# Kernel tuning notes

Measured on AMD Instinct MI355X. Metric: run time of the kernel, lower is better.

## Reference

```python
import jax, jax.numpy as jnp
import numpy as np

B, S = 2, 1024
V, H = 32000, 1024
NH, NKV = 16, 8
HD = H // NH          # 64
L = 8
I = 4 * H             # 4096
EPS = 1e-6
THETA = 10000.0
NEG = -1e9


def setup_inputs() -> dict:
    key = jax.random.key(0)
    ks = jax.random.split(key, 12)
    std = 0.02
    f = lambda k, shape: jax.random.normal(k, shape, jnp.float32) * std
    return {
        "input_ids": jax.random.randint(ks[0], (B, S), 0, V, dtype=jnp.int32),
        "embed": f(ks[1], (V, H)),
        "Wq": f(ks[2], (L, H, NH * HD)),
        "Wk": f(ks[3], (L, H, NKV * HD)),
        "Wv": f(ks[4], (L, H, NKV * HD)),
        "Wo": f(ks[5], (L, NH * HD, H)),
        "Wg": f(ks[6], (L, H, I)),
        "Wu": f(ks[7], (L, H, I)),
        "Wd": f(ks[8], (L, I, H)),
        "ln1": jnp.ones((L, H), jnp.float32),
        "ln2": jnp.ones((L, H), jnp.float32),
        "norm_w": jnp.ones((H,), jnp.float32),
        "lm_head": f(ks[9], (H, V)),
    }


def _rmsnorm(x, w):
    var = jnp.mean(x * x, axis=-1, keepdims=True)
    return x * jax.lax.rsqrt(var + EPS) * w


def _rotate_half(x):
    x1, x2 = jnp.split(x, 2, axis=-1)
    return jnp.concatenate((-x2, x1), axis=-1)


def reference(input_ids, embed, Wq, Wk, Wv, Wo, Wg, Wu, Wd, ln1, ln2, norm_w, lm_head):
    # RoPE tables [S, HD] (freqs duplicated, matching cat((freqs, freqs)))
    inv_freq = 1.0 / (THETA ** (jnp.arange(0, HD, 2, dtype=jnp.float32) / HD))
    t = jnp.arange(S, dtype=jnp.float32)
    freqs = t[:, None] * inv_freq[None, :]
    emb = jnp.concatenate((freqs, freqs), axis=-1)
    cos = jnp.cos(emb)[None, None]  # [1,1,S,HD]
    sin = jnp.sin(emb)[None, None]
    # causal mask [S, S]
    mask = jnp.where(jnp.tril(jnp.ones((S, S), bool)), 0.0, NEG).astype(jnp.float32)

    def layer(h, p):
        wq, wk, wv, wo, wg, wu, wd, g1, g2 = p
        x = _rmsnorm(h, g1)
        q = (x @ wq).reshape(B, S, NH, HD).transpose(0, 2, 1, 3)   # [B,NH,S,HD]
        k = (x @ wk).reshape(B, S, NKV, HD).transpose(0, 2, 1, 3)  # [B,NKV,S,HD]
        v = (x @ wv).reshape(B, S, NKV, HD).transpose(0, 2, 1, 3)
        q = q * cos + _rotate_half(q) * sin
        k = k * cos + _rotate_half(k) * sin
        rep = NH // NKV
        k = jnp.repeat(k, rep, axis=1)  # GQA repeat_interleave
        v = jnp.repeat(v, rep, axis=1)
        scores = jnp.einsum("bhqd,bhkd->bhqk", q, k) / np.sqrt(HD) + mask
        probs = jax.nn.softmax(scores, axis=-1)
        o = jnp.einsum("bhqk,bhkd->bhqd", probs, v)
        o = o.transpose(0, 2, 1, 3).reshape(B, S, NH * HD)
        h = h + o @ wo
        x = _rmsnorm(h, g2)
        h = h + (jax.nn.silu(x @ wg) * (x @ wu)) @ wd
        return h, None

    h = embed[input_ids]  # [B,S,H]
    h, _ = jax.lax.scan(layer, h, (Wq, Wk, Wv, Wo, Wg, Wu, Wd, ln1, ln2))
    h = _rmsnorm(h, norm_w)
    return h @ lm_head  # logits [B,S,V]
```

## Files before the change

### kernel.cpp

```cpp
#include <hip/hip_runtime.h>


typedef unsigned short u16;
typedef __bf16  bf16x8 __attribute__((ext_vector_type(8)));
typedef unsigned short u16x8 __attribute__((ext_vector_type(8)));
typedef float   f32x4  __attribute__((ext_vector_type(4)));

#define DEV static __device__ __forceinline__

constexpr int NB  = 2;
constexpr int S   = 1024;
constexpr int NT  = NB * S;
constexpr int H   = 1024;
constexpr int NH  = 16;
constexpr int NKV = 8;
constexpr int HD  = 64;
constexpr int NL  = 8;
constexpr int FF  = 4096;
constexpr int V   = 32000;
constexpr int QKVW = 2048;

DEV float b2f(u16 x) { return __uint_as_float(((unsigned)x) << 16); }
DEV u16   f2b(float f) {
  unsigned i = __float_as_uint(f);
  return (u16)((i + 0x7fffu + ((i >> 16) & 1u)) >> 16);
}

DEV void gload16(const void* g, void* l) {
  __builtin_amdgcn_global_load_lds(
      (const __attribute__((address_space(1))) void*)g,
      (__attribute__((address_space(3))) void*)l, 16, 0, 0);
}

DEV bf16x8 ld128(const u16* p) { return *reinterpret_cast<const bf16x8*>(p); }

template <int EPI>
__global__ __launch_bounds__(512, 2) void gemm256_k(
    const u16* __restrict__ A, int lda,
    const u16* __restrict__ Bt, int ldb,
    void* __restrict__ C, int ldc, int K)
{
  __shared__ __align__(16) u16 Asm[4][256 * 32];
  __shared__ __align__(16) u16 Bsm[4][256 * 32];

  const int tid  = threadIdx.x;
  const int lane = tid & 63;
  const int lrow = lane & 15;
  const int g    = lane >> 4;
  const int wid  = tid >> 6;
  const int wm   = wid >> 2, wn = wid & 3;

  int flat = blockIdx.y * gridDim.x + blockIdx.x;
  const int cpx = (gridDim.x * gridDim.y) >> 3;
  flat = (flat & 7) * cpx + (flat >> 3);
  const int bx = flat % gridDim.x;
  const int by = flat / gridDim.x;

  const int r0   = tid >> 2, pp = tid & 3;
  const int row1 = 128 + (tid >> 2);
  const int p0 = pp ^ ((r0 ^ (r0 >> 2)) & 3);
  const int p1 = pp ^ ((row1 ^ (row1 >> 2)) & 3);
  const u16* aS0 = A  + (size_t)(bx * 256 + r0)   * lda + p0 * 8;
  const u16* aS1 = A  + (size_t)(bx * 256 + row1) * lda + p1 * 8;
  const u16* bS0 = Bt + (size_t)(by * 256 + r0)   * ldb + p0 * 8;
  const u16* bS1 = Bt + (size_t)(by * 256 + row1) * ldb + p1 * 8;
  const int aB0 = tid * 16, aB1 = (512 + tid) * 16;

  int aOff[8], bOff[4];
  #pragma unroll
  for (int fm = 0; fm < 8; fm++) {
    const int r = wm * 128 + fm * 16 + lrow;
    aOff[fm] = r * 32 + (g ^ ((r ^ (r >> 2)) & 3)) * 8;
  }
  #pragma unroll
  for (int fn = 0; fn < 4; fn++) {
    const int r = wn * 64 + fn * 16 + lrow;
    bOff[fn] = r * 32 + (g ^ ((r ^ (r >> 2)) & 3)) * 8;
  }

  f32x4 acc[8][4] = {};
  const int ntk = K / 32;

  #pragma unroll
  for (int ts = 0; ts < 3; ts++) {
    const long kt = (long)ts * 32;
    gload16(aS0 + kt, (char*)Asm[ts] + aB0);
    gload16(bS0 + kt, (char*)Bsm[ts] + aB0);
    gload16(aS1 + kt, (char*)Asm[ts] + aB1);
    gload16(bS1 + kt, (char*)Bsm[ts] + aB1);
  }
  asm volatile("s_waitcnt vmcnt(8)" ::: "memory");
  __builtin_amdgcn_s_barrier();

#define KTILE(VMW, STG)                                                         \
  {                                                                             \
    const int rs = t & 3, ss = (t + 3) & 3;                                     \
    const long kt = (long)(t + 3) * 32;                                         \
    bf16x8 af[4], bf[4];                                                        \
    _Pragma("unroll") for (int i = 0; i < 4; i++) bf[i] = ld128(&Bsm[rs][bOff[i]]); \
    _Pragma("unroll") for (int i = 0; i < 4; i++) af[i] = ld128(&Asm[rs][aOff[i]]); \
    if (STG) { gload16(aS0 + kt, (char*)Asm[ss] + aB0);                         \
               gload16(bS0 + kt, (char*)Bsm[ss] + aB0); }                       \
    __builtin_amdgcn_s_barrier();                                               \
    asm volatile("s_waitcnt lgkmcnt(0)" ::: "memory");                          \
    __builtin_amdgcn_sched_barrier(0);                                          \
    __builtin_amdgcn_s_setprio(1);                                              \
    _Pragma("unroll") for (int m = 0; m < 4; m++)                               \
      _Pragma("unroll") for (int n = 0; n < 4; n++)                             \
        acc[m][n] = __builtin_amdgcn_mfma_f32_16x16x32_bf16(af[m], bf[n], acc[m][n], 0, 0, 0); \
    __builtin_amdgcn_s_setprio(0);                                              \
    __builtin_amdgcn_s_barrier();                                               \
    _Pragma("unroll") for (int i = 0; i < 4; i++) af[i] = ld128(&Asm[rs][aOff[4 + i]]); \
    if (STG) { gload16(aS1 + kt, (char*)Asm[ss] + aB1);                         \
               gload16(bS1 + kt, (char*)Bsm[ss] + aB1); }                       \
    __builtin_amdgcn_s_barrier();                                               \
    asm volatile("s_waitcnt lgkmcnt(0)" ::: "memory");                          \
    __builtin_amdgcn_sched_barrier(0);                                          \
    __builtin_amdgcn_s_setprio(1);                                              \
    _Pragma("unroll") for (int m = 0; m < 4; m++)                               \
      _Pragma("unroll") for (int n = 0; n < 4; n++)                             \
        acc[4 + m][n] = __builtin_amdgcn_mfma_f32_16x16x32_bf16(af[m], bf[n], acc[4 + m][n], 0, 0, 0); \
    __builtin_amdgcn_s_setprio(0);                                              \
    VMW;                                                                        \
    __builtin_amdgcn_sched_barrier(0);                                          \
    __builtin_amdgcn_s_barrier();                                               \
  }

  {
    int t = 0;
    for (; t < ntk - 3; ++t) KTILE(asm volatile("s_waitcnt vmcnt(8)" ::: "memory"), true);
    KTILE(asm volatile("s_waitcnt vmcnt(4)" ::: "memory"), false); ++t;
    KTILE(asm volatile("s_waitcnt vmcnt(0)" ::: "memory"), false); ++t;
    KTILE((void)0, false);
  }
#undef KTILE

  if (EPI == 2) {
    #pragma unroll
    for (int fm = 0; fm < 8; fm++) {
      #pragma unroll
      for (int fp = 0; fp < 2; fp++) {
        #pragma unroll
        for (int r = 0; r < 4; r++) {
          const size_t row = bx * 256 + wm * 128 + fm * 16 + g * 4 + r;
          const int nb = by * 256 + wn * 64 + fp * 32;
          const int oc = (nb >> 5) * 16 + lrow;
          const float gg = acc[fm][2 * fp][r];
          const float uu = acc[fm][2 * fp + 1][r];
          ((u16*)C)[row * ldc + oc] = f2b(gg / (1.f + __expf(-gg)) * uu);
        }
      }
    }
  } else {
    #pragma unroll
    for (int fm = 0; fm < 8; fm++) {
      #pragma unroll
      for (int fn = 0; fn < 4; fn++) {
        #pragma unroll
        for (int r = 0; r < 4; r++) {
          const size_t row = bx * 256 + wm * 128 + fm * 16 + g * 4 + r;
          const size_t col = by * 256 + wn * 64 + fn * 16 + lrow;
          ((float*)C)[row * ldc + col] = acc[fm][fn][r];
        }
      }
    }
  }
}

template <int BM, int BN, int WM, int WN, int EPI>
__global__ __launch_bounds__(256) void gemm_k(
    const u16* __restrict__ A, int lda,
    const u16* __restrict__ Bt, int ldb,
    void* __restrict__ C, int ldc,
    const float2* __restrict__ tab, int K)
{
  __shared__ __align__(16) u16 As[BM * 32];
  __shared__ __align__(16) u16 Bs[BN * 32];

  const int tid  = threadIdx.x;
  const int lane = tid & 63;
  const int lrow = lane & 15;
  const int kb   = lane >> 4;
  const int w    = tid >> 6;
  const int wm   = w / WN, wn = w % WN;
  constexpr int WR = BM / WM, WC = BN / WN;
  constexpr int FM = WR / 16, FN = WC / 16;

  const u16* Ap = A + blockIdx.x * BM * lda;
  const u16* Bp = Bt + blockIdx.y * BN * ldb;

  f32x4 acc[FM][FN] = {};

  for (int k0 = 0; k0 < K; k0 += 32) {
    #pragma unroll
    for (int i = 0; i < (BM * 4) / 256; i++) {
      const int c = i * 256 + tid;
      gload16(Ap + (c >> 2) * lda + k0 + (c & 3) * 8, (char*)As + c * 16);
    }
    #pragma unroll
    for (int i = 0; i < (BN * 4) / 256; i++) {
      const int c = i * 256 + tid;
      gload16(Bp + (c >> 2) * ldb + k0 + (c & 3) * 8, (char*)Bs + c * 16);
    }
    __syncthreads();

    bf16x8 af[FM], bfv[FN];
    #pragma unroll
    for (int fm = 0; fm < FM; fm++)
      af[fm] = *reinterpret_cast<const bf16x8*>(As + (wm * WR + fm * 16 + lrow) * 32 + kb * 8);
    #pragma unroll
    for (int fn = 0; fn < FN; fn++)
      bfv[fn] = *reinterpret_cast<const bf16x8*>(Bs + (wn * WC + fn * 16 + lrow) * 32 + kb * 8);

    #pragma unroll
    for (int fm = 0; fm < FM; fm++) {
      #pragma unroll
      for (int fn = 0; fn < FN; fn++) {
        acc[fm][fn] = __builtin_amdgcn_mfma_f32_16x16x32_bf16(af[fm], bfv[fn], acc[fm][fn], 0, 0, 0);
      }
    }
    __syncthreads();
  }

  if (EPI == 4) {
    const int colb = blockIdx.y * BN + wn * WC;
    const int head = colb >> 6;
    const float qs = (head < 16) ? 0.125f : 1.0f;
    #pragma unroll
    for (int fm = 0; fm < FM; fm++) {
      #pragma unroll
      for (int r = 0; r < 4; r++) {
        const int row = blockIdx.x * BM + wm * WR + fm * 16 + kb * 4 + r;
        if (head >= 24) {
          #pragma unroll
          for (int fn = 0; fn < FN; fn++)
            ((u16*)C)[row * ldc + colb + fn * 16 + lrow] = f2b(acc[fm][fn][r]);
        } else {
          const int s = row & (S - 1);
          #pragma unroll
          for (int fp = 0; fp < 2; fp++) {
            const int d = fp * 16 + lrow;
            const float2 cs = tab[s * 32 + d];
            const float x1 = acc[fm][fp][r];
            const float x2 = acc[fm][fp + 2][r];
            ((u16*)C)[row * ldc + colb + d]      = f2b((x1 * cs.x - x2 * cs.y) * qs);
            ((u16*)C)[row * ldc + colb + d + 32] = f2b((x2 * cs.x + x1 * cs.y) * qs);
          }
        }
      }
    }
  } else {
    #pragma unroll
    for (int fm = 0; fm < FM; fm++) {
      #pragma unroll
      for (int fn = 0; fn < FN; fn++) {
        #pragma unroll
        for (int r = 0; r < 4; r++) {
          const int row = blockIdx.x * BM + wm * WR + fm * 16 + kb * 4 + r;
          const int col = blockIdx.y * BN + wn * WC + fn * 16 + lrow;
          ((u16*)C)[row * ldc + col] = f2b(acc[fm][fn][r]);
        }
      }
    }
  }
}

__global__ __launch_bounds__(256) void transpose_k(
    const float* __restrict__ W, u16* __restrict__ WT, int K, int N, int rmode,
    size_t wstride, size_t tstride)
{
  __shared__ float t[32][33];
  const float* Wp = W + (size_t)blockIdx.z * wstride;
  u16* WTp = WT + (size_t)blockIdx.z * tstride;
  const int k0 = blockIdx.x * 32, n0 = blockIdx.y * 32;
  const int tx = threadIdx.x & 31, ty = threadIdx.x >> 5;
  #pragma unroll
  for (int i = 0; i < 32; i += 8)
    t[ty + i][tx] = Wp[(size_t)(k0 + ty + i) * N + (n0 + tx)];
  __syncthreads();
  #pragma unroll
  for (int i = 0; i < 32; i += 8) {
    const int n = n0 + ty + i;
    const int orow = (rmode == 0) ? n : ((n >> 4) * 32 + (n & 15) + ((rmode == 2) ? 16 : 0));
    WTp[(size_t)orow * K + (k0 + tx)] = f2b(t[tx][ty + i]);
  }
}

__global__ __launch_bounds__(256) void embed_k(
    const int* __restrict__ ids, const float* __restrict__ E, float* __restrict__ h)
{
  const int t = blockIdx.x;
  const int id = ids[t];
  ((float4*)(h + t * H))[threadIdx.x] = ((const float4*)(E + (size_t)id * H))[threadIdx.x];
}

__global__ __launch_bounds__(256) void rmsnorm_k(
    const float* __restrict__ h, const float* __restrict__ w, u16* __restrict__ x)
{
  const int row = blockIdx.x;
  const float4 hv = ((const float4*)(h + row * H))[threadIdx.x];
  float s = hv.x * hv.x + hv.y * hv.y + hv.z * hv.z + hv.w * hv.w;
  #pragma unroll
  for (int off = 32; off; off >>= 1) s += __shfl_xor(s, off, 64);
  __shared__ float red[4];
  if ((threadIdx.x & 63) == 0) red[threadIdx.x >> 6] = s;
  __syncthreads();
  s = red[0] + red[1] + red[2] + red[3];
  const float scale = rsqrtf(s * (1.f / H) + 1e-6f);
  const float4 wv = ((const float4*)w)[threadIdx.x];
  ushort4 ov;
  ov.x = f2b(hv.x * scale * wv.x);
  ov.y = f2b(hv.y * scale * wv.y);
  ov.z = f2b(hv.z * scale * wv.z);
  ov.w = f2b(hv.w * scale * wv.w);
  ((ushort4*)(x + row * H))[threadIdx.x] = ov;
}

__global__ __launch_bounds__(256) void addnorm_k(
    float* __restrict__ h, const u16* __restrict__ dl,
    const float* __restrict__ w, u16* __restrict__ x)
{
  const int row = blockIdx.x;
  float4 hv = ((const float4*)(h + row * H))[threadIdx.x];
  const ushort4 dv = ((const ushort4*)(dl + row * H))[threadIdx.x];
  hv.x += b2f(dv.x); hv.y += b2f(dv.y); hv.z += b2f(dv.z); hv.w += b2f(dv.w);
  ((float4*)(h + row * H))[threadIdx.x] = hv;
  float s = hv.x * hv.x + hv.y * hv.y + hv.z * hv.z + hv.w * hv.w;
  #pragma unroll
  for (int off = 32; off; off >>= 1) s += __shfl_xor(s, off, 64);
  __shared__ float red[4];
  if ((threadIdx.x & 63) == 0) red[threadIdx.x >> 6] = s;
  __syncthreads();
  s = red[0] + red[1] + red[2] + red[3];
  const float scale = rsqrtf(s * (1.f / H) + 1e-6f);
  const float4 wv = ((const float4*)w)[threadIdx.x];
  ushort4 ov;
  ov.x = f2b(hv.x * scale * wv.x);
  ov.y = f2b(hv.y * scale * wv.y);
  ov.z = f2b(hv.z * scale * wv.z);
  ov.w = f2b(hv.w * scale * wv.w);
  ((ushort4*)(x + row * H))[threadIdx.x] = ov;
}

__global__ __launch_bounds__(256) void ropetab_k(float2* __restrict__ tab)
{
  const int idx = blockIdx.x * 256 + threadIdx.x;
  const int s = idx >> 5, d = idx & 31;
  const float ang = s * powf(10000.f, -(2.f * d) / 64.f);
  float sn, cs;
  sincosf(ang, &sn, &cs);
  tab[idx] = make_float2(cs, sn);
}

__global__ __launch_bounds__(256) void fattn_k(
    const u16* __restrict__ qkv, u16* __restrict__ o)
{
  __shared__ __align__(16) u16 Ks[64 * 64];
  __shared__ __align__(16) u16 Vt[64 * 72];
  __shared__ __align__(16) u16 Pw[4][16 * 64];

  const int tid  = threadIdx.x;
  const int lane = tid & 63;
  const int lrow = lane & 15;
  const int g    = lane >> 4;
  const int w    = tid >> 6;

  const int bid = blockIdx.x;
  const int j   = bid >> 3;
  const int bh  = (bid & 7) * 4 + (j & 3);
  const int bx  = 15 - (j >> 2);
  const int b = bh >> 4, hh = bh & 15, kh = hh >> 1;
  const int q0 = bx * 64;

  bf16x8 aq[2];
  {
    const int qrow = q0 + w * 16 + lrow;
    const u16* qp = qkv + (size_t)(b * S + qrow) * QKVW + hh * 64 + g * 8;
    aq[0] = *reinterpret_cast<const bf16x8*>(qp);
    aq[1] = *reinterpret_cast<const bf16x8*>(qp + 32);
  }

  f32x4 oacc[4] = {};
  float mrow[4], lsum[4];
  #pragma unroll
  for (int r = 0; r < 4; r++) { mrow[r] = -1e30f; lsum[r] = 0.f; }

  const int nt = bx + 1;
  for (int t = 0; t < nt; t++) {
    const int kv0 = t * 64;
    __syncthreads();

    #pragma unroll
    for (int i = 0; i < 2; i++) {
      const int c = i * 256 + tid;
      const int r = c >> 3, p = c & 7;
      gload16(qkv + (size_t)(b * S + kv0 + r) * QKVW + 1024 + kh * 64 + ((p ^ (r & 7)) * 8),
              (char*)Ks + c * 16);
    }
    u16x8 vreg[2];
    #pragma unroll
    for (int i = 0; i < 2; i++) {
      const int c = i * 256 + tid;
      const int k = c >> 3, dch = c & 7;
      vreg[i] = *reinterpret_cast<const u16x8*>(
          qkv + (size_t)(b * S + kv0 + k) * QKVW + 1536 + kh * 64 + dch * 8);
    }
    #pragma unroll
    for (int i = 0; i < 2; i++) {
      const int c = i * 256 + tid;
      const int k = c >> 3, d0 = (c & 7) * 8;
      #pragma unroll
      for (int j2 = 0; j2 < 8; j2++) {
        const int d = d0 + j2;
        Vt[d * 72 + (((k >> 3) ^ (d >> 3)) * 8) + (k & 7)] = vreg[i][j2];
      }
    }
    __syncthreads();

    f32x4 sacc[4] = {};
    #pragma unroll
    for (int n = 0; n < 4; n++) {
      const int row = n * 16 + lrow;
      #pragma unroll
      for (int k2 = 0; k2 < 2; k2++) {
        const bf16x8 bk = *reinterpret_cast<const bf16x8*>(
            Ks + row * 64 + (((k2 * 4 + g) ^ (row & 7)) * 8));
        sacc[n] = __builtin_amdgcn_mfma_f32_16x16x32_bf16(aq[k2], bk, sacc[n], 0, 0, 0);
      }
    }

    float rmv[4];
    #pragma unroll
    for (int r = 0; r < 4; r++) {
      const int qglob = q0 + w * 16 + g * 4 + r;
      float rm = -1e30f;
      #pragma unroll
      for (int n = 0; n < 4; n++) {
        const int kg = kv0 + n * 16 + lrow;
        if (kg > qglob) sacc[n][r] = -1e30f;
        rm = fmaxf(rm, sacc[n][r]);
      }
      #pragma unroll
      for (int mk = 1; mk < 16; mk <<= 1) rm = fmaxf(rm, __shfl_xor(rm, mk, 64));
      rmv[r] = rm;
    }

    int need = 0;
    #pragma unroll
    for (int r = 0; r < 4; r++) need |= (rmv[r] > mrow[r] + 8.f) ? 1 : 0;
    if (__any(need)) {
      #pragma unroll
      for (int r = 0; r < 4; r++) {
        const float mnew  = fmaxf(mrow[r], rmv[r]);
        const float scale = __expf(mrow[r] - mnew);
        mrow[r] = mnew;
        lsum[r] *= scale;
        #pragma unroll
        for (int dt = 0; dt < 4; dt++) oacc[dt][r] *= scale;
      }
    }

    #pragma unroll
    for (int r = 0; r < 4; r++) {
      float rs = 0.f;
      u16 pb[4];
      #pragma unroll
      for (int n = 0; n < 4; n++) {
        const float p = __expf(sacc[n][r] - mrow[r]);
        rs += p;
        pb[n] = f2b(p);
      }
      #pragma unroll
      for (int mk = 1; mk < 16; mk <<= 1) rs += __shfl_xor(rs, mk, 64);
      lsum[r] += rs;
      const int ql = g * 4 + r;
      #pragma unroll
      for (int n = 0; n < 4; n++) {
        const int k = n * 16 + lrow;
        Pw[w][ql * 64 + (((k >> 3) ^ (ql & 7)) * 8) + (k & 7)] = pb[n];
      }
    }

    #pragma unroll
    for (int k2 = 0; k2 < 2; k2++) {
      const bf16x8 pa = *reinterpret_cast<const bf16x8*>(
          &Pw[w][lrow * 64 + (((k2 * 4 + g) ^ (lrow & 7)) * 8)]);
      #pragma unroll
      for (int dt = 0; dt < 4; dt++) {
        const int d = dt * 16 + lrow;
        const bf16x8 vb = *reinterpret_cast<const bf16x8*>(
            &Vt[d * 72 + (((k2 * 4 + g) ^ (d >> 3)) * 8)]);
        oacc[dt] = __builtin_amdgcn_mfma_f32_16x16x32_bf16(pa, vb, oacc[dt], 0, 0, 0);
      }
    }
  }

  #pragma unroll
  for (int dt = 0; dt < 4; dt++) {
    #pragma unroll
    for (int r = 0; r < 4; r++) {
      const int qrow = q0 + w * 16 + g * 4 + r;
      o[(size_t)(b * S + qrow) * H + hh * 64 + dt * 16 + lrow] =
          f2b(oacc[dt][r] / lsum[r]);
    }
  }
}

extern "C" void kernel_launch(void* const* d_in, const int* in_sizes, int n_in,
                              void* d_out, int out_size, void* d_ws, size_t ws_size,
                              hipStream_t stream)
{
  const int*   ids  = (const int*)d_in[0];
  const float* EW   = (const float*)d_in[1];
  const float* Wq   = (const float*)d_in[2];
  const float* Wk   = (const float*)d_in[3];
  const float* Wv   = (const float*)d_in[4];
  const float* Wo   = (const float*)d_in[5];
  const float* Wg   = (const float*)d_in[6];
  const float* Wu   = (const float*)d_in[7];
  const float* Wd   = (const float*)d_in[8];
  const float* ln1  = (const float*)d_in[9];
  const float* ln2  = (const float*)d_in[10];
  const float* nw   = (const float*)d_in[11];
  const float* lmw  = (const float*)d_in[12];
  float* out = (float*)d_out;

  const size_t MB = 1u << 20;
  char* ws = (char*)d_ws;
  float*  h   = (float*)(ws);
  u16*    x   = (u16*)(ws + 8 * MB);
  u16*    qkv = (u16*)(ws + 12 * MB);
  u16*    o   = (u16*)(ws + 20 * MB);
  u16*    dl  = (u16*)(ws + 24 * MB);
  u16*    ub  = (u16*)(ws + 28 * MB);
  float2* tab = (float2*)(ws + 44 * MB);
  char*   wb  = ws + 45 * MB;

  const size_t sqkv = (size_t)QKVW * H;
  const size_t swo  = (size_t)H * H;
  const size_t sgu  = (size_t)2 * FF * H;
  const size_t swd  = (size_t)H * FF;

  const bool full = ws_size >= 349 * MB;
  if (!full && ws_size < 108 * MB) return;

  u16 *wqkvT, *woT, *wguT, *wdT, *lmT;
  if (full) {
    wqkvT = (u16*)wb;
    woT   = wqkvT + NL * sqkv;
    wguT  = woT + NL * swo;
    wdT   = wguT + NL * sgu;
    lmT   = wdT + NL * swd;
  } else {
    wqkvT = (u16*)wb;
    woT   = wqkvT + sqkv;
    wguT  = woT + swo;
    wdT   = wguT + sgu;
    lmT   = (u16*)wb;
  }

  auto xpose = [&](int l0, int lz, bool dense) {
    const size_t tq = dense ? sqkv : 0, to = dense ? swo : 0;
    const size_t tg = dense ? sgu : 0,  td = dense ? swd : 0;
    transpose_k<<<dim3(H / 32, H / 32, lz), 256, 0, stream>>>(
        Wq + (size_t)l0 * H * H, wqkvT + (size_t)l0 * tq, H, H, 0, (size_t)H * H, tq);
    transpose_k<<<dim3(H / 32, 512 / 32, lz), 256, 0, stream>>>(
        Wk + (size_t)l0 * H * 512, wqkvT + (size_t)l0 * tq + (size_t)1024 * H, H, 512, 0,
        (size_t)H * 512, tq);
    transpose_k<<<dim3(H / 32, 512 / 32, lz), 256, 0, stream>>>(
        Wv + (size_t)l0 * H * 512, wqkvT + (size_t)l0 * tq + (size_t)1536 * H, H, 512, 0,
        (size_t)H * 512, tq);
    transpose_k<<<dim3(H / 32, H / 32, lz), 256, 0, stream>>>(
        Wo + (size_t)l0 * H * H, woT + (size_t)l0 * to, H, H, 0, (size_t)H * H, to);
    transpose_k<<<dim3(H / 32, FF / 32, lz), 256, 0, stream>>>(
        Wg + (size_t)l0 * H * FF, wguT + (size_t)l0 * tg, H, FF, 1, (size_t)H * FF, tg);
    transpose_k<<<dim3(H / 32, FF / 32, lz), 256, 0, stream>>>(
        Wu + (size_t)l0 * H * FF, wguT + (size_t)l0 * tg, H, FF, 2, (size_t)H * FF, tg);
    transpose_k<<<dim3(FF / 32, H / 32, lz), 256, 0, stream>>>(
        Wd + (size_t)l0 * FF * H, wdT + (size_t)l0 * td, FF, H, 0, (size_t)FF * H, td);
  };

  embed_k<<<NT, 256, 0, stream>>>(ids, EW, h);
  ropetab_k<<<(S * 32) / 256, 256, 0, stream>>>(tab);

  if (full) {
    xpose(0, NL, true);
    transpose_k<<<dim3(H / 32, V / 32, 1), 256, 0, stream>>>(lmw, lmT, H, V, 0, 0, 0);
  }

  rmsnorm_k<<<NT, 256, 0, stream>>>(h, ln1, x);

  for (int l = 0; l < NL; l++) {
    if (!full) xpose(l, 1, false);
    u16* pq = wqkvT + (full ? (size_t)l * sqkv : 0);
    u16* po = woT   + (full ? (size_t)l * swo  : 0);
    u16* pg = wguT  + (full ? (size_t)l * sgu  : 0);
    u16* pd = wdT   + (full ? (size_t)l * swd  : 0);

    gemm_k<64, 128, 2, 2, 4><<<dim3(NT / 64, QKVW / 128), 256, 0, stream>>>(
        x, H, pq, H, qkv, QKVW, tab, H);
    fattn_k<<<dim3(512), 256, 0, stream>>>(qkv, o);
    gemm_k<64, 64, 2, 2, 0><<<dim3(NT / 64, H / 64), 256, 0, stream>>>(
        o, H, po, H, dl, H, nullptr, H);
    addnorm_k<<<NT, 256, 0, stream>>>(h, dl, ln2 + l * H, x);

    gemm256_k<2><<<dim3(NT / 256, (2 * FF) / 256), 512, 0, stream>>>(
        x, H, pg, H, ub, FF, H);
    gemm_k<64, 64, 2, 2, 0><<<dim3(NT / 64, H / 64), 256, 0, stream>>>(
        ub, FF, pd, FF, dl, H, nullptr, FF);
    const float* nxt = (l + 1 < NL) ? (ln1 + (l + 1) * H) : nw;
    addnorm_k<<<NT, 256, 0, stream>>>(h, dl, nxt, x);
  }

  if (!full)
    transpose_k<<<dim3(H / 32, V / 32, 1), 256, 0, stream>>>(lmw, lmT, H, V, 0, 0, 0);
  gemm256_k<3><<<dim3(NT / 256, V / 256), 512, 0, stream>>>(
      x, H, lmT, H, out, V, H);
}
```

Before: 1.987 ms.

## Multi-stage prefetch pipeline with swizzled LDS in generic gemm_k

```diff
diff --git a/kernel.cpp b/kernel.cpp
--- a/kernel.cpp
+++ b/kernel.cpp
@@ -33,6 +33,15 @@
 }
 
 DEV bf16x8 ld128(const u16* p) { return *reinterpret_cast<const bf16x8*>(p); }
+
+template <int N> DEV void waitvm() {
+  if constexpr (N == 0)      asm volatile("s_waitcnt vmcnt(0)" ::: "memory");
+  else if constexpr (N == 2) asm volatile("s_waitcnt vmcnt(2)" ::: "memory");
+  else if constexpr (N == 3) asm volatile("s_waitcnt vmcnt(3)" ::: "memory");
+  else if constexpr (N == 4) asm volatile("s_waitcnt vmcnt(4)" ::: "memory");
+  else if constexpr (N == 6) asm volatile("s_waitcnt vmcnt(6)" ::: "memory");
+  else                       asm volatile("s_waitcnt vmcnt(8)" ::: "memory");
+}
 
 template <int EPI>
 __global__ __launch_bounds__(512, 2) void gemm256_k(
@@ -174,8 +183,12 @@
     void* __restrict__ C, int ldc,
     const float2* __restrict__ tab, int K)
 {
-  __shared__ __align__(16) u16 As[BM * 32];
-  __shared__ __align__(16) u16 Bs[BN * 32];
+  constexpr int LA = (BM * 4) / 256;
+  constexpr int LB = (BN * 4) / 256;
+  constexpr int LT = LA + LB;
+
+  __shared__ __align__(16) u16 Asm[4][BM * 32];
+  __shared__ __align__(16) u16 Bsm[4][BN * 32];
 
   const int tid  = threadIdx.x;
   const int lane = tid & 63;
@@ -186,41 +199,82 @@
   constexpr int WR = BM / WM, WC = BN / WN;
   constexpr int FM = WR / 16, FN = WC / 16;
 
-  const u16* Ap = A + blockIdx.x * BM * lda;
-  const u16* Bp = Bt + blockIdx.y * BN * ldb;
+  const u16* aS[LA];
+  const u16* bS[LB];
+  #pragma unroll
+  for (int i = 0; i < LA; i++) {
+    const int row = (i * 256 + tid) >> 2, pp = tid & 3;
+    const int p = pp ^ ((row ^ (row >> 2)) & 3);
+    aS[i] = A + (size_t)(blockIdx.x * BM + row) * lda + p * 8;
+  }
+  #pragma unroll
+  for (int i = 0; i < LB; i++) {
+    const int row = (i * 256 + tid) >> 2, pp = tid & 3;
+    const int p = pp ^ ((row ^ (row >> 2)) & 3);
+    bS[i] = Bt + (size_t)(blockIdx.y * BN + row) * ldb + p * 8;
+  }
+
+  int aOff[FM], bOff[FN];
+  #pragma unroll
+  for (int fm = 0; fm < FM; fm++) {
+    const int r = wm * WR + fm * 16 + lrow;
+    aOff[fm] = r * 32 + (kb ^ ((r ^ (r >> 2)) & 3)) * 8;
+  }
+  #pragma unroll
+  for (int fn = 0; fn < FN; fn++) {
+    const int r = wn * WC + fn * 16 + lrow;
+    bOff[fn] = r * 32 + (kb ^ ((r ^ (r >> 2)) & 3)) * 8;
+  }
 
   f32x4 acc[FM][FN] = {};
-
-  for (int k0 = 0; k0 < K; k0 += 32) {
-    #pragma unroll
-    for (int i = 0; i < (BM * 4) / 256; i++) {
-      const int c = i * 256 + tid;
-      gload16(Ap + (c >> 2) * lda + k0 + (c & 3) * 8, (char*)As + c * 16);
-    }
-    #pragma unroll
-    for (int i = 0; i < (BN * 4) / 256; i++) {
-      const int c = i * 256 + tid;
-      gload16(Bp + (c >> 2) * ldb + k0 + (c & 3) * 8, (char*)Bs + c * 16);
-    }
-    __syncthreads();
-
-    bf16x8 af[FM], bfv[FN];
-    #pragma unroll
-    for (int fm = 0; fm < FM; fm++)
-      af[fm] = *reinterpret_cast<const bf16x8*>(As + (wm * WR + fm * 16 + lrow) * 32 + kb * 8);
-    #pragma unroll
-    for (int fn = 0; fn < FN; fn++)
-      bfv[fn] = *reinterpret_cast<const bf16x8*>(Bs + (wn * WC + fn * 16 + lrow) * 32 + kb * 8);
-
-    #pragma unroll
-    for (int fm = 0; fm < FM; fm++) {
-      #pragma unroll
-      for (int fn = 0; fn < FN; fn++) {
-        acc[fm][fn] = __builtin_amdgcn_mfma_f32_16x16x32_bf16(af[fm], bfv[fn], acc[fm][fn], 0, 0, 0);
-      }
-    }
-    __syncthreads();
-  }
+  const int ntk = K / 32;
+
+  #pragma unroll
+  for (int ts = 0; ts < 3; ts++) {
+    #pragma unroll
+    for (int i = 0; i < LA; i++)
+      gload16(aS[i] + ts * 32, (char*)Asm[ts] + (i * 256 + tid) * 16);
+    #pragma unroll
+    for (int i = 0; i < LB; i++)
+      gload16(bS[i] + ts * 32, (char*)Bsm[ts] + (i * 256 + tid) * 16);
+  }
+  waitvm<2 * LT>();
+  __builtin_amdgcn_s_barrier();
+
+#define SKTILE(VMW, STG)                                                        \
+  {                                                                             \
+    const int rs = t & 3, ss = (t + 3) & 3;                                     \
+    const long kt = (long)(t + 3) * 32;                                         \
+    bf16x8 af[FM], bf[FN];                                                      \
+    _Pragma("unroll") for (int i = 0; i < FN; i++) bf[i] = ld128(&Bsm[rs][bOff[i]]); \
+    _Pragma("unroll") for (int i = 0; i < FM; i++) af[i] = ld128(&Asm[rs][aOff[i]]); \
+    if (STG) {                                                                  \
+      _Pragma("unroll") for (int i = 0; i < LA; i++)                            \
+        gload16(aS[i] + kt, (char*)Asm[ss] + (i * 256 + tid) * 16);             \
+      _Pragma("unroll") for (int i = 0; i < LB; i++)                            \
+        gload16(bS[i] + kt, (char*)Bsm[ss] + (i * 256 + tid) * 16);             \
+    }                                                                           \
+    __builtin_amdgcn_s_barrier();                                               \
+    asm volatile("s_waitcnt lgkmcnt(0)" ::: "memory");                          \
+    __builtin_amdgcn_sched_barrier(0);                                          \
+    __builtin_amdgcn_s_setprio(1);                                              \
+    _Pragma("unroll") for (int m = 0; m < FM; m++)                              \
+      _Pragma("unroll") for (int n = 0; n < FN; n++)                            \
+        acc[m][n] = __builtin_amdgcn_mfma_f32_16x16x32_bf16(af[m], bf[n], acc[m][n], 0, 0, 0); \
+    __builtin_amdgcn_s_setprio(0);                                              \
+    VMW;                                                                        \
+    __builtin_amdgcn_sched_barrier(0);                                          \
+    __builtin_amdgcn_s_barrier();                                               \
+  }
+
+  {
+    int t = 0;
+    for (; t < ntk - 3; ++t) SKTILE(waitvm<2 * LT>(), true);
+    SKTILE(waitvm<LT>(), false); ++t;
+    SKTILE(waitvm<0>(), false); ++t;
+    SKTILE((void)0, false);
+  }
+#undef SKTILE
 
   if (EPI == 4) {
     const int colb = blockIdx.y * BN + wn * WC;
```

Result: faster. 1.810 ms (median of 2 runs) (-8.9%).
